# Kernel tuning notes

Measured on AMD Instinct MI355X. Metric: run time of the kernel, lower is better.

## Reference

```python
import jax, jax.numpy as jnp
import numpy as np

D_MODEL = 1024
NUM_HEADS = 16
HEAD_DIM = D_MODEL // NUM_HEADS


def setup_inputs() -> dict:
    key = jax.random.key(0)
    ks = jax.random.split(key, 11)
    B, S = 4, 2048
    scale = 1.0 / np.sqrt(D_MODEL)
    inp = {
        'q': jax.random.normal(ks[0], (B, S, D_MODEL), jnp.float32),
        'k': jax.random.normal(ks[1], (B, S, D_MODEL), jnp.float32),
        'v': jax.random.normal(ks[2], (B, S, D_MODEL), jnp.float32),
        'Wq': jax.random.normal(ks[3], (D_MODEL, D_MODEL), jnp.float32) * scale,
        'bq': jnp.zeros((D_MODEL,), jnp.float32),
        'Wk': jax.random.normal(ks[4], (D_MODEL, D_MODEL), jnp.float32) * scale,
        'bk': jnp.zeros((D_MODEL,), jnp.float32),
        'Wv': jax.random.normal(ks[5], (D_MODEL, D_MODEL), jnp.float32) * scale,
        'bv': jnp.zeros((D_MODEL,), jnp.float32),
        'Wo': jax.random.normal(ks[6], (D_MODEL, D_MODEL), jnp.float32) * scale,
        'bo': jnp.zeros((D_MODEL,), jnp.float32),
    }
    return inp


def _split_heads(x):
    B, S, _ = x.shape
    return x.reshape(B, S, NUM_HEADS, HEAD_DIM).transpose(0, 2, 1, 3)  # [B,H,S,Dh]


def reference(q, k, v, Wq, bq, Wk, bk, Wv, bv, Wo, bo):
    Q = _split_heads(q @ Wq.T + bq)
    K = _split_heads(k @ Wk.T + bk)
    V = _split_heads(v @ Wv.T + bv)
    scores = jnp.einsum('bhqd,bhkd->bhqk', Q, K) / jnp.sqrt(jnp.float32(HEAD_DIM))
    attn = jax.nn.softmax(scores, axis=-1)
    out = jnp.einsum('bhqk,bhkd->bhqd', attn, V)  # [B,H,S,Dh]
    B, _, S, _ = out.shape
    out = out.transpose(0, 2, 1, 3).reshape(B, S, D_MODEL)
    return out @ Wo.T + bo
```

## Files before the change

kernel.cpp:

```cpp
#include <hip/hip_runtime.h>
#include <hip/hip_bf16.h>

#define DMODEL 1024
#define NHEADS 16
#define HDIM 64

typedef __bf16 bf16_t;
typedef __bf16 bf16x8 __attribute__((ext_vector_type(8)));
typedef float  f32x4  __attribute__((ext_vector_type(4)));
typedef float  f32x16 __attribute__((ext_vector_type(16)));

__device__ __forceinline__ bf16_t f2bf(float f) {
    unsigned int u = __builtin_bit_cast(unsigned int, f);
    u += 0x7FFF + ((u >> 16) & 1);
    unsigned short h = (unsigned short)(u >> 16);
    return __builtin_bit_cast(bf16_t, h);
}

__device__ __forceinline__ unsigned cvt_pk_bf16(float lo, float hi) {
    unsigned r;
    asm("v_cvt_pk_bf16_f32 %0, %1, %2" : "=v"(r) : "v"(lo), "v"(hi));
    return r;
}

__device__ __forceinline__ void gld_lds16(const bf16_t* g, bf16_t* l) {
    __builtin_amdgcn_global_load_lds(
        (const __attribute__((address_space(1))) unsigned int*)g,
        (__attribute__((address_space(3))) unsigned int*)l, 16, 0, 0);
}

__global__ __launch_bounds__(256) void cast_all(const float* __restrict__ Wq,
                                                const float* __restrict__ Wk,
                                                const float* __restrict__ Wv,
                                                const float* __restrict__ Wo,
                                                const float* __restrict__ q,
                                                const float* __restrict__ k,
                                                const float* __restrict__ v,
                                                bf16_t* __restrict__ Wall,
                                                bf16_t* __restrict__ qb,
                                                bf16_t* __restrict__ kb,
                                                bf16_t* __restrict__ vb,
                                                int nw, int na) {
    const int y = blockIdx.y;
    const float* s;
    bf16_t* d;
    int n;
    if (y == 0)      { s = Wq; d = Wall;               n = nw; }
    else if (y == 1) { s = Wk; d = Wall + (size_t)nw;  n = nw; }
    else if (y == 2) { s = Wv; d = Wall + 2 * (size_t)nw; n = nw; }
    else if (y == 3) { s = Wo; d = Wall + 3 * (size_t)nw; n = nw; }
    else if (y == 4) { s = q;  d = qb; n = na; }
    else if (y == 5) { s = k;  d = kb; n = na; }
    else             { s = v;  d = vb; n = na; }
    int i = blockIdx.x * blockDim.x + threadIdx.x;
    int stride = gridDim.x * blockDim.x;
    for (int idx = i * 4; idx < n; idx += stride * 4) {
        float4 vv = *reinterpret_cast<const float4*>(s + idx);
        uint2 u;
        u.x = cvt_pk_bf16(vv.x, vv.y);
        u.y = cvt_pk_bf16(vv.z, vv.w);
        *reinterpret_cast<uint2*>(d + idx) = u;
    }
}

__global__ __launch_bounds__(256) void gemm_qkv(const bf16_t* __restrict__ qb,
                                                const bf16_t* __restrict__ kb,
                                                const bf16_t* __restrict__ vb,
                                                const bf16_t* __restrict__ Wall,
                                                const float* __restrict__ bq,
                                                const float* __restrict__ bk,
                                                const float* __restrict__ bv,
                                                bf16_t* __restrict__ Qp,
                                                bf16_t* __restrict__ Kf,
                                                bf16_t* __restrict__ Vf,
                                                int M, float qscale, int S) {
    __shared__ bf16_t smemU[16384];
    const int K = DMODEL, N = DMODEL;
    const int z = blockIdx.z;
    const bf16_t* Ab = (z == 0) ? qb : (z == 1) ? kb : vb;
    const bf16_t* W = Wall + (size_t)z * DMODEL * DMODEL;
    const float* bias = (z == 0) ? bq : (z == 1) ? bk : bv;

    const int m0 = blockIdx.x * 128;
    const int n0 = blockIdx.y * 128;
    const int tid = threadIdx.x;
    const int wave = tid >> 6, lane = tid & 63;
    const int wm = wave >> 1, wn = wave & 1;
    const int lr = lane & 15, lg = lane >> 4;
    const int srow = lane >> 2, scol = (lane & 3) * 8;

    const bool swp = (z == 1);
    const int xo = (swp ? wn : wm) * 64;
    const int yo = (swp ? wm : wn) * 64;

    f32x4 acc[4][4];
#pragma unroll
    for (int i = 0; i < 4; ++i)
#pragma unroll
        for (int j = 0; j < 4; ++j) acc[i][j] = (f32x4){0.f, 0.f, 0.f, 0.f};

#pragma unroll
    for (int i = 0; i < 2; ++i) {
        int c = wave * 2 + i;
        gld_lds16(Ab + (size_t)(m0 + c * 16 + srow) * K + scol, smemU + c * 512);
        gld_lds16(W + (size_t)(n0 + c * 16 + srow) * K + scol, smemU + 8192 + c * 512);
    }
    asm volatile("s_waitcnt vmcnt(0)" ::: "memory");
    __syncthreads();

    const int nk = K / 32;
    for (int t = 0; t < nk; ++t) {
        const int cur = t & 1, nxt = cur ^ 1;
        const int ktn = (t + 1) * 32;
        if (t + 1 < nk) {
#pragma unroll
            for (int i = 0; i < 2; ++i) {
                int c = wave * 2 + i;
                gld_lds16(Ab + (size_t)(m0 + c * 16 + srow) * K + ktn + scol,
                          smemU + nxt * 4096 + c * 512);
                gld_lds16(W + (size_t)(n0 + c * 16 + srow) * K + ktn + scol,
                          smemU + 8192 + nxt * 4096 + c * 512);
            }
        }
        const bf16_t* Xs = smemU + (swp ? 8192 : 0) + cur * 4096;
        const bf16_t* Ys = smemU + (swp ? 0 : 8192) + cur * 4096;
        bf16x8 X[4], Y[4];
#pragma unroll
        for (int i = 0; i < 4; ++i)
            X[i] = *reinterpret_cast<const bf16x8*>(&Xs[(xo + i * 16 + lr) * 32 + lg * 8]);
#pragma unroll
        for (int j = 0; j < 4; ++j)
            Y[j] = *reinterpret_cast<const bf16x8*>(&Ys[(yo + j * 16 + lr) * 32 + lg * 8]);
#pragma unroll
        for (int i = 0; i < 4; ++i)
#pragma unroll
            for (int j = 0; j < 4; ++j)
                acc[i][j] = __builtin_amdgcn_mfma_f32_16x16x32_bf16(X[i], Y[j], acc[i][j], 0, 0, 0);
        asm volatile("s_waitcnt vmcnt(0)" ::: "memory");
        __syncthreads();
    }

    if (z == 0) {
#pragma unroll
        for (int i = 0; i < 4; ++i) {
            int row = m0 + wm * 64 + i * 16 + lg * 4;
#pragma unroll
            for (int j = 0; j < 4; ++j) {
                int col = n0 + wn * 64 + j * 16 + lr;
                float bv_ = bias[col];
#pragma unroll
                for (int r = 0; r < 4; ++r)
                    Qp[(size_t)(row + r) * N + col] = f2bf((acc[i][j][r] + bv_) * qscale);
            }
        }
    } else {
        const int key0 = m0 + wm * 64;
        const int b_ = key0 / S;
        const int t_ = (key0 % S) >> 6;
        const int h  = (n0 + wn * 64) >> 6;
        bf16_t* bounce = smemU + wave * 4096;
        if (z == 1) {
#pragma unroll
            for (int i = 0; i < 4; ++i) {
                int d0 = i * 16 + lg * 4;
                float4 bv4 = *reinterpret_cast<const float4*>(bias + h * 64 + d0);
#pragma unroll
                for (int j = 0; j < 4; ++j) {
                    uint2 u;
                    u.x = cvt_pk_bf16(acc[i][j][0] + bv4.x, acc[i][j][1] + bv4.y);
                    u.y = cvt_pk_bf16(acc[i][j][2] + bv4.z, acc[i][j][3] + bv4.w);
                    int key5 = (j & 1) * 16 + lr;
                    int off = ((j >> 1) * 4 + i) * 512 + key5 * 8 + (lg >> 1) * 256 + (lg & 1) * 4;
                    *reinterpret_cast<uint2*>(bounce + off) = u;
                }
            }
        } else {
#pragma unroll
            for (int j = 0; j < 4; ++j) {
                int dl = (j & 1) * 16 + lr;
                int gd = j >> 1;
                float bv_ = bias[h * 64 + j * 16 + lr];
#pragma unroll
                for (int i = 0; i < 4; ++i) {
                    uint2 u;
                    u.x = cvt_pk_bf16(acc[i][j][0] + bv_, acc[i][j][1] + bv_);
                    u.y = cvt_pk_bf16(acc[i][j][2] + bv_, acc[i][j][3] + bv_);
                    int off = (gd * 4 + i) * 512 + dl * 8 + (lg >> 1) * 256 + (lg & 1) * 4;
                    *reinterpret_cast<uint2*>(bounce + off) = u;
                }
            }
        }
        bf16_t* gout = ((z == 1) ? Kf : Vf)
                     + (size_t)(b_ * NHEADS + h) * ((size_t)S * HDIM) + (size_t)(t_ * 8) * 512;
#pragma unroll
        for (int c = 0; c < 8; ++c) {
            bf16x8 vv = *reinterpret_cast<const bf16x8*>(bounce + c * 512 + lane * 8);
            *reinterpret_cast<bf16x8*>(gout + c * 512 + lane * 8) = vv;
        }
    }
}

__global__ __launch_bounds__(256) void gemm_out(const bf16_t* __restrict__ Ab,
                                                const bf16_t* __restrict__ W,
                                                const float* __restrict__ bias,
                                                float* __restrict__ Cout,
                                                int M, int N, int K) {
    __shared__ bf16_t Asmem[2][128 * 32];
    __shared__ bf16_t Bsmem[2][128 * 32];
    const int m0 = blockIdx.x * 128;
    const int n0 = blockIdx.y * 128;
    const int tid = threadIdx.x;
    const int wave = tid >> 6, lane = tid & 63;
    const int wm = wave >> 1, wn = wave & 1;
    const int lr = lane & 15, lg = lane >> 4;
    const int srow = lane >> 2, scol = (lane & 3) * 8;

    f32x4 acc[4][4];
#pragma unroll
    for (int mi = 0; mi < 4; ++mi)
#pragma unroll
        for (int ni = 0; ni < 4; ++ni) acc[mi][ni] = (f32x4){0.f, 0.f, 0.f, 0.f};

#pragma unroll
    for (int i = 0; i < 2; ++i) {
        int c = wave * 2 + i;
        gld_lds16(Ab + (size_t)(m0 + c * 16 + srow) * K + scol, &Asmem[0][c * 512]);
        gld_lds16(W + (size_t)(n0 + c * 16 + srow) * K + scol, &Bsmem[0][c * 512]);
    }
    asm volatile("s_waitcnt vmcnt(0)" ::: "memory");
    __syncthreads();

    const int nk = K / 32;
    for (int t = 0; t < nk; ++t) {
        const int cur = t & 1, nxt = cur ^ 1;
        const int ktn = (t + 1) * 32;
        if (t + 1 < nk) {
#pragma unroll
            for (int i = 0; i < 2; ++i) {
                int c = wave * 2 + i;
                gld_lds16(Ab + (size_t)(m0 + c * 16 + srow) * K + ktn + scol, &Asmem[nxt][c * 512]);
                gld_lds16(W + (size_t)(n0 + c * 16 + srow) * K + ktn + scol, &Bsmem[nxt][c * 512]);
            }
        }
        bf16x8 af[4], bfr[4];
#pragma unroll
        for (int mi = 0; mi < 4; ++mi)
            af[mi] = *reinterpret_cast<const bf16x8*>(&Asmem[cur][(wm * 64 + mi * 16 + lr) * 32 + lg * 8]);
#pragma unroll
        for (int ni = 0; ni < 4; ++ni)
            bfr[ni] = *reinterpret_cast<const bf16x8*>(&Bsmem[cur][(wn * 64 + ni * 16 + lr) * 32 + lg * 8]);
#pragma unroll
        for (int mi = 0; mi < 4; ++mi)
#pragma unroll
            for (int ni = 0; ni < 4; ++ni)
                acc[mi][ni] = __builtin_amdgcn_mfma_f32_16x16x32_bf16(af[mi], bfr[ni], acc[mi][ni], 0, 0, 0);
        asm volatile("s_waitcnt vmcnt(0)" ::: "memory");
        __syncthreads();
    }

#pragma unroll
    for (int mi = 0; mi < 4; ++mi) {
        int row = m0 + wm * 64 + mi * 16 + lg * 4;
#pragma unroll
        for (int ni = 0; ni < 4; ++ni) {
            int col = n0 + wn * 64 + ni * 16 + lr;
            float bv = bias[col];
#pragma unroll
            for (int r = 0; r < 4; ++r)
                Cout[(size_t)(row + r) * N + col] = acc[mi][ni][r] + bv;
        }
    }
}

__global__ __launch_bounds__(256, 2) void attn_kernel(const bf16_t* __restrict__ Qp,
                                                      const bf16_t* __restrict__ KfG,
                                                      const bf16_t* __restrict__ VfG,
                                                      bf16_t* __restrict__ AO, int S) {
    const int tid = threadIdx.x;
    const int wave = tid >> 6, lane = tid & 63;
    const int ql = lane & 31;
    const int hi = lane >> 5;
    const int bh = blockIdx.x;
    const int b = bh >> 4, h = bh & 15;
    const int qt = blockIdx.y;
    const size_t base = ((size_t)b * S) * DMODEL + (size_t)h * HDIM;
    const size_t fbase = (size_t)bh * ((size_t)S * HDIM);

    const int qrow = qt * 128 + wave * 32 + ql;
    bf16x8 qf[4];
#pragma unroll
    for (int kc = 0; kc < 4; ++kc)
        qf[kc] = *reinterpret_cast<const bf16x8*>(Qp + base + (size_t)qrow * DMODEL + kc * 16 + hi * 8);

    f32x16 o0{}, o1{};
    float l_r = 0.f;

    const bf16_t* Kf = KfG + fbase;
    const bf16_t* Vf = VfG + fbase;
    const int le = lane * 8;

    const int NT = S / 64;
    for (int t = 0; t < NT; ++t) {
        const bf16_t* kt = Kf + t * 4096;
        const bf16_t* vt = Vf + t * 4096;
        bf16x8 kf0[4], kf1[4], vf0[4], vf1[4];
#pragma unroll
        for (int c = 0; c < 4; ++c) {
            kf0[c] = *reinterpret_cast<const bf16x8*>(kt + c * 512 + le);
            kf1[c] = *reinterpret_cast<const bf16x8*>(kt + 2048 + c * 512 + le);
            vf0[c] = *reinterpret_cast<const bf16x8*>(vt + c * 512 + le);
            vf1[c] = *reinterpret_cast<const bf16x8*>(vt + 2048 + c * 512 + le);
        }

        f32x16 s0{}, s1{};
        __builtin_amdgcn_s_setprio(1);
#pragma unroll
        for (int kc = 0; kc < 4; ++kc)
            s0 = __builtin_amdgcn_mfma_f32_32x32x16_bf16(kf0[kc], qf[kc], s0, 0, 0, 0);
#pragma unroll
        for (int kc = 0; kc < 4; ++kc)
            s1 = __builtin_amdgcn_mfma_f32_32x32x16_bf16(kf1[kc], qf[kc], s1, 0, 0, 0);
        __builtin_amdgcn_s_setprio(0);

#pragma unroll
        for (int r = 0; r < 16; ++r) {
            s0[r] = __builtin_amdgcn_exp2f(s0[r]);
            s1[r] = __builtin_amdgcn_exp2f(s1[r]);
        }
        float a4[8];
#pragma unroll
        for (int j = 0; j < 8; ++j)
            a4[j] = (s0[2 * j] + s0[2 * j + 1]) + (s1[2 * j] + s1[2 * j + 1]);
        float a2[4];
#pragma unroll
        for (int j = 0; j < 4; ++j) a2[j] = a4[2 * j] + a4[2 * j + 1];
        l_r += (a2[0] + a2[1]) + (a2[2] + a2[3]);

        unsigned w[8][2];
#pragma unroll
        for (int j = 0; j < 4; ++j) {
            w[j][0] = cvt_pk_bf16(s0[4 * j], s0[4 * j + 1]);
            w[j][1] = cvt_pk_bf16(s0[4 * j + 2], s0[4 * j + 3]);
            w[4 + j][0] = cvt_pk_bf16(s1[4 * j], s1[4 * j + 1]);
            w[4 + j][1] = cvt_pk_bf16(s1[4 * j + 2], s1[4 * j + 3]);
        }

#pragma unroll
        for (int kq = 0; kq < 4; ++kq) {
            unsigned own0 = hi ? w[2 * kq + 1][0] : w[2 * kq][0];
            unsigned own1 = hi ? w[2 * kq + 1][1] : w[2 * kq][1];
            unsigned y0 = hi ? w[2 * kq][0] : w[2 * kq + 1][0];
            unsigned y1 = hi ? w[2 * kq][1] : w[2 * kq + 1][1];
            y0 = (unsigned)__shfl_xor((int)y0, 32, 64);
            y1 = (unsigned)__shfl_xor((int)y1, 32, 64);
            union { unsigned u[4]; bf16x8 v; } pb;
            pb.u[0] = hi ? y0 : own0;
            pb.u[1] = hi ? y1 : own1;
            pb.u[2] = hi ? own0 : y0;
            pb.u[3] = hi ? own1 : y1;
            __builtin_amdgcn_s_setprio(1);
            o0 = __builtin_amdgcn_mfma_f32_32x32x16_bf16(vf0[kq], pb.v, o0, 0, 0, 0);
            o1 = __builtin_amdgcn_mfma_f32_32x32x16_bf16(vf1[kq], pb.v, o1, 0, 0, 0);
            __builtin_amdgcn_s_setprio(0);
        }
    }

    float l_all = l_r + __shfl_xor(l_r, 32, 64);
    float inv = 1.f / l_all;
    bf16_t* Ao = AO + base + (size_t)qrow * DMODEL;
#pragma unroll
    for (int j = 0; j < 4; ++j) {
        uint2 u0, u1;
        u0.x = cvt_pk_bf16(o0[4 * j] * inv, o0[4 * j + 1] * inv);
        u0.y = cvt_pk_bf16(o0[4 * j + 2] * inv, o0[4 * j + 3] * inv);
        *reinterpret_cast<uint2*>(Ao + 8 * j + 4 * hi) = u0;
        u1.x = cvt_pk_bf16(o1[4 * j] * inv, o1[4 * j + 1] * inv);
        u1.y = cvt_pk_bf16(o1[4 * j + 2] * inv, o1[4 * j + 3] * inv);
        *reinterpret_cast<uint2*>(Ao + 32 + 8 * j + 4 * hi) = u1;
    }
}

extern "C" void kernel_launch(void* const* d_in, const int* in_sizes, int n_in,
                              void* d_out, int out_size, void* d_ws, size_t ws_size,
                              hipStream_t stream) {
    const float* q  = (const float*)d_in[0];
    const float* k  = (const float*)d_in[1];
    const float* v  = (const float*)d_in[2];
    const float* Wq = (const float*)d_in[3];
    const float* bq = (const float*)d_in[4];
    const float* Wk = (const float*)d_in[5];
    const float* bk = (const float*)d_in[6];
    const float* Wv = (const float*)d_in[7];
    const float* bv = (const float*)d_in[8];
    const float* Wo = (const float*)d_in[9];
    const float* bo = (const float*)d_in[10];

    const int M = in_sizes[0] / DMODEL;
    const int S = 2048;
    const int B = M / S;

    bf16_t* ws  = (bf16_t*)d_ws;
    const size_t WSZ = (size_t)DMODEL * DMODEL;
    const size_t MSZ = (size_t)M * DMODEL;
    bf16_t* Wqb = ws;
    bf16_t* Wob = Wqb + 3 * WSZ;
    bf16_t* Qp  = Wob + WSZ;
    bf16_t* Kf  = Qp + MSZ;
    bf16_t* Vf  = Kf + MSZ;
    bf16_t* shX = Vf + MSZ;
    bf16_t* qb  = (bf16_t*)d_out;
    bf16_t* kb  = qb + MSZ;
    bf16_t* vb  = shX;
    bf16_t* AO  = shX;

    cast_all<<<dim3(2048, 7), 256, 0, stream>>>(Wq, Wk, Wv, Wo, q, k, v,
                                                ws, qb, kb, vb,
                                                DMODEL * DMODEL, M * DMODEL);

    const float qscale = 0.125f * 1.44269504088896f;
    gemm_qkv<<<dim3(M / 128, DMODEL / 128, 3), 256, 0, stream>>>(
        qb, kb, vb, Wqb, bq, bk, bv, Qp, Kf, Vf, M, qscale, S);

    attn_kernel<<<dim3(B * NHEADS, S / 128), 256, 0, stream>>>(Qp, Kf, Vf, AO, S);

    gemm_out<<<dim3(M / 128, DMODEL / 128), 256, 0, stream>>>(
        AO, Wob, bo, (float*)d_out, M, DMODEL, DMODEL);
}
```

Measured before the change: 226.8 us.

## Process two query row tiles per wave to reuse K/V fragments

Each wave now handles 64 query rows (two 32-row groups) instead of 32, so every K and V fragment loaded from global memory feeds twice as many MFMAs. The grid's query-tile dimension is halved to match, and V loads move into the PV loop to limit register pressure. This cuts K/V load traffic per unit of compute, but doubles the accumulator registers, which may reduce occupancy under launch_bounds(256,2) or cause spills. It also leaves only 512 blocks.

```diff
diff --git a/kernel.cpp b/kernel.cpp
--- a/kernel.cpp
+++ b/kernel.cpp
@@ -286,14 +286,17 @@
     const size_t base = ((size_t)b * S) * DMODEL + (size_t)h * HDIM;
     const size_t fbase = (size_t)bh * ((size_t)S * HDIM);
 
-    const int qrow = qt * 128 + wave * 32 + ql;
-    bf16x8 qf[4];
-#pragma unroll
-    for (int kc = 0; kc < 4; ++kc)
-        qf[kc] = *reinterpret_cast<const bf16x8*>(Qp + base + (size_t)qrow * DMODEL + kc * 16 + hi * 8);
-
-    f32x16 o0{}, o1{};
-    float l_r = 0.f;
+    const int qrowA = qt * 256 + wave * 32 + ql;
+    const int qrowB = qrowA + 128;
+    bf16x8 qfA[4], qfB[4];
+#pragma unroll
+    for (int kc = 0; kc < 4; ++kc) {
+        qfA[kc] = *reinterpret_cast<const bf16x8*>(Qp + base + (size_t)qrowA * DMODEL + kc * 16 + hi * 8);
+        qfB[kc] = *reinterpret_cast<const bf16x8*>(Qp + base + (size_t)qrowB * DMODEL + kc * 16 + hi * 8);
+    }
+
+    f32x16 oA0{}, oA1{}, oB0{}, oB1{};
+    float lA = 0.f, lB = 0.f;
 
     const bf16_t* Kf = KfG + fbase;
     const bf16_t* Vf = VfG + fbase;
@@ -303,80 +306,124 @@
     for (int t = 0; t < NT; ++t) {
         const bf16_t* kt = Kf + t * 4096;
         const bf16_t* vt = Vf + t * 4096;
-        bf16x8 kf0[4], kf1[4], vf0[4], vf1[4];
+
+        bf16x8 kf0[4], kf1[4];
 #pragma unroll
         for (int c = 0; c < 4; ++c) {
             kf0[c] = *reinterpret_cast<const bf16x8*>(kt + c * 512 + le);
             kf1[c] = *reinterpret_cast<const bf16x8*>(kt + 2048 + c * 512 + le);
-            vf0[c] = *reinterpret_cast<const bf16x8*>(vt + c * 512 + le);
-            vf1[c] = *reinterpret_cast<const bf16x8*>(vt + 2048 + c * 512 + le);
-        }
-
-        f32x16 s0{}, s1{};
+        }
+        f32x16 sA0{}, sA1{}, sB0{}, sB1{};
         __builtin_amdgcn_s_setprio(1);
 #pragma unroll
-        for (int kc = 0; kc < 4; ++kc)
-            s0 = __builtin_amdgcn_mfma_f32_32x32x16_bf16(kf0[kc], qf[kc], s0, 0, 0, 0);
-#pragma unroll
-        for (int kc = 0; kc < 4; ++kc)
-            s1 = __builtin_amdgcn_mfma_f32_32x32x16_bf16(kf1[kc], qf[kc], s1, 0, 0, 0);
+        for (int kc = 0; kc < 4; ++kc) {
+            sA0 = __builtin_amdgcn_mfma_f32_32x32x16_bf16(kf0[kc], qfA[kc], sA0, 0, 0, 0);
+            sB0 = __builtin_amdgcn_mfma_f32_32x32x16_bf16(kf0[kc], qfB[kc], sB0, 0, 0, 0);
+            sA1 = __builtin_amdgcn_mfma_f32_32x32x16_bf16(kf1[kc], qfA[kc], sA1, 0, 0, 0);
+            sB1 = __builtin_amdgcn_mfma_f32_32x32x16_bf16(kf1[kc], qfB[kc], sB1, 0, 0, 0);
+        }
         __builtin_amdgcn_s_setprio(0);
 
 #pragma unroll
         for (int r = 0; r < 16; ++r) {
-            s0[r] = __builtin_amdgcn_exp2f(s0[r]);
-            s1[r] = __builtin_amdgcn_exp2f(s1[r]);
-        }
-        float a4[8];
-#pragma unroll
-        for (int j = 0; j < 8; ++j)
-            a4[j] = (s0[2 * j] + s0[2 * j + 1]) + (s1[2 * j] + s1[2 * j + 1]);
-        float a2[4];
-#pragma unroll
-        for (int j = 0; j < 4; ++j) a2[j] = a4[2 * j] + a4[2 * j + 1];
-        l_r += (a2[0] + a2[1]) + (a2[2] + a2[3]);
-
-        unsigned w[8][2];
+            sA0[r] = __builtin_amdgcn_exp2f(sA0[r]);
+            sA1[r] = __builtin_amdgcn_exp2f(sA1[r]);
+            sB0[r] = __builtin_amdgcn_exp2f(sB0[r]);
+            sB1[r] = __builtin_amdgcn_exp2f(sB1[r]);
+        }
+        {
+            float a4[8], b4[8];
+#pragma unroll
+            for (int j = 0; j < 8; ++j) {
+                a4[j] = (sA0[2 * j] + sA0[2 * j + 1]) + (sA1[2 * j] + sA1[2 * j + 1]);
+                b4[j] = (sB0[2 * j] + sB0[2 * j + 1]) + (sB1[2 * j] + sB1[2 * j + 1]);
+            }
+            float a2[4], b2[4];
+#pragma unroll
+            for (int j = 0; j < 4; ++j) {
+                a2[j] = a4[2 * j] + a4[2 * j + 1];
+                b2[j] = b4[2 * j] + b4[2 * j + 1];
+            }
+            lA += (a2[0] + a2[1]) + (a2[2] + a2[3]);
+            lB += (b2[0] + b2[1]) + (b2[2] + b2[3]);
+        }
+
+        unsigned wA[8][2], wB[8][2];
 #pragma unroll
         for (int j = 0; j < 4; ++j) {
-            w[j][0] = cvt_pk_bf16(s0[4 * j], s0[4 * j + 1]);
-            w[j][1] = cvt_pk_bf16(s0[4 * j + 2], s0[4 * j + 3]);
-            w[4 + j][0] = cvt_pk_bf16(s1[4 * j], s1[4 * j + 1]);
-            w[4 + j][1] = cvt_pk_bf16(s1[4 * j + 2], s1[4 * j + 3]);
+            wA[j][0] = cvt_pk_bf16(sA0[4 * j], sA0[4 * j + 1]);
+            wA[j][1] = cvt_pk_bf16(sA0[4 * j + 2], sA0[4 * j + 3]);
+            wA[4 + j][0] = cvt_pk_bf16(sA1[4 * j], sA1[4 * j + 1]);
+            wA[4 + j][1] = cvt_pk_bf16(sA1[4 * j + 2], sA1[4 * j + 3]);
+            wB[j][0] = cvt_pk_bf16(sB0[4 * j], sB0[4 * j + 1]);
+            wB[j][1] = cvt_pk_bf16(sB0[4 * j + 2], sB0[4 * j + 3]);
+            wB[4 + j][0] = cvt_pk_bf16(sB1[4 * j], sB1[4 * j + 1]);
+            wB[4 + j][1] = cvt_pk_bf16(sB1[4 * j + 2], sB1[4 * j + 3]);
         }
 
 #pragma unroll
         for (int kq = 0; kq < 4; ++kq) {
-            unsigned own0 = hi ? w[2 * kq + 1][0] : w[2 * kq][0];
-            unsigned own1 = hi ? w[2 * kq + 1][1] : w[2 * kq][1];
-            unsigned y0 = hi ? w[2 * kq][0] : w[2 * kq + 1][0];
-            unsigned y1 = hi ? w[2 * kq][1] : w[2 * kq + 1][1];
-            y0 = (unsigned)__shfl_xor((int)y0, 32, 64);
-            y1 = (unsigned)__shfl_xor((int)y1, 32, 64);
-            union { unsigned u[4]; bf16x8 v; } pb;
-            pb.u[0] = hi ? y0 : own0;
-            pb.u[1] = hi ? y1 : own1;
-            pb.u[2] = hi ? own0 : y0;
-            pb.u[3] = hi ? own1 : y1;
+            bf16x8 vf0 = *reinterpret_cast<const bf16x8*>(vt + kq * 512 + le);
+            bf16x8 vf1 = *reinterpret_cast<const bf16x8*>(vt + 2048 + kq * 512 + le);
+            unsigned oA0_ = hi ? wA[2 * kq + 1][0] : wA[2 * kq][0];
+            unsigned oA1_ = hi ? wA[2 * kq + 1][1] : wA[2 * kq][1];
+            unsigned yA0 = hi ? wA[2 * kq][0] : wA[2 * kq + 1][0];
+            unsigned yA1 = hi ? wA[2 * kq][1] : wA[2 * kq + 1][1];
+            yA0 = (unsigned)__shfl_xor((int)yA0, 32, 64);
+            yA1 = (unsigned)__shfl_xor((int)yA1, 32, 64);
+            unsigned oB0_ = hi ? wB[2 * kq + 1][0] : wB[2 * kq][0];
+            unsigned oB1_ = hi ? wB[2 * kq + 1][1] : wB[2 * kq][1];
+            unsigned yB0 = hi ? wB[2 * kq][0] : wB[2 * kq + 1][0];
+            unsigned yB1 = hi ? wB[2 * kq][1] : wB[2 * kq + 1][1];
+            yB0 = (unsigned)__shfl_xor((int)yB0, 32, 64);
+            yB1 = (unsigned)__shfl_xor((int)yB1, 32, 64);
+            union { unsigned u[4]; bf16x8 v; } pbA, pbB;
+            pbA.u[0] = hi ? yA0 : oA0_;
+            pbA.u[1] = hi ? yA1 : oA1_;
+            pbA.u[2] = hi ? oA0_ : yA0;
+            pbA.u[3] = hi ? oA1_ : yA1;
+            pbB.u[0] = hi ? yB0 : oB0_;
+            pbB.u[1] = hi ? yB1 : oB1_;
+            pbB.u[2] = hi ? oB0_ : yB0;
+            pbB.u[3] = hi ? oB1_ : yB1;
             __builtin_amdgcn_s_setprio(1);
-            o0 = __builtin_amdgcn_mfma_f32_32x32x16_bf16(vf0[kq], pb.v, o0, 0, 0, 0);
-            o1 = __builtin_amdgcn_mfma_f32_32x32x16_bf16(vf1[kq], pb.v, o1, 0, 0, 0);
+            oA0 = __builtin_amdgcn_mfma_f32_32x32x16_bf16(vf0, pbA.v, oA0, 0, 0, 0);
+            oB0 = __builtin_amdgcn_mfma_f32_32x32x16_bf16(vf0, pbB.v, oB0, 0, 0, 0);
+            oA1 = __builtin_amdgcn_mfma_f32_32x32x16_bf16(vf1, pbA.v, oA1, 0, 0, 0);
+            oB1 = __builtin_amdgcn_mfma_f32_32x32x16_bf16(vf1, pbB.v, oB1, 0, 0, 0);
             __builtin_amdgcn_s_setprio(0);
         }
     }
 
-    float l_all = l_r + __shfl_xor(l_r, 32, 64);
-    float inv = 1.f / l_all;
-    bf16_t* Ao = AO + base + (size_t)qrow * DMODEL;
-#pragma unroll
-    for (int j = 0; j < 4; ++j) {
-        uint2 u0, u1;
-        u0.x = cvt_pk_bf16(o0[4 * j] * inv, o0[4 * j + 1] * inv);
-        u0.y = cvt_pk_bf16(o0[4 * j + 2] * inv, o0[4 * j + 3] * inv);
-        *reinterpret_cast<uint2*>(Ao + 8 * j + 4 * hi) = u0;
-        u1.x = cvt_pk_bf16(o1[4 * j] * inv, o1[4 * j + 1] * inv);
-        u1.y = cvt_pk_bf16(o1[4 * j + 2] * inv, o1[4 * j + 3] * inv);
-        *reinterpret_cast<uint2*>(Ao + 32 + 8 * j + 4 * hi) = u1;
+    {
+        float l_all = lA + __shfl_xor(lA, 32, 64);
+        float inv = 1.f / l_all;
+        bf16_t* Ao = AO + base + (size_t)qrowA * DMODEL;
+#pragma unroll
+        for (int j = 0; j < 4; ++j) {
+            uint2 u0, u1;
+            u0.x = cvt_pk_bf16(oA0[4 * j] * inv, oA0[4 * j + 1] * inv);
+            u0.y = cvt_pk_bf16(oA0[4 * j + 2] * inv, oA0[4 * j + 3] * inv);
+            *reinterpret_cast<uint2*>(Ao + 8 * j + 4 * hi) = u0;
+            u1.x = cvt_pk_bf16(oA1[4 * j] * inv, oA1[4 * j + 1] * inv);
+            u1.y = cvt_pk_bf16(oA1[4 * j + 2] * inv, oA1[4 * j + 3] * inv);
+            *reinterpret_cast<uint2*>(Ao + 32 + 8 * j + 4 * hi) = u1;
+        }
+    }
+    {
+        float l_all = lB + __shfl_xor(lB, 32, 64);
+        float inv = 1.f / l_all;
+        bf16_t* Ao = AO + base + (size_t)qrowB * DMODEL;
+#pragma unroll
+        for (int j = 0; j < 4; ++j) {
+            uint2 u0, u1;
+            u0.x = cvt_pk_bf16(oB0[4 * j] * inv, oB0[4 * j + 1] * inv);
+            u0.y = cvt_pk_bf16(oB0[4 * j + 2] * inv, oB0[4 * j + 3] * inv);
+            *reinterpret_cast<uint2*>(Ao + 8 * j + 4 * hi) = u0;
+            u1.x = cvt_pk_bf16(oB1[4 * j] * inv, oB1[4 * j + 1] * inv);
+            u1.y = cvt_pk_bf16(oB1[4 * j + 2] * inv, oB1[4 * j + 3] * inv);
+            *reinterpret_cast<uint2*>(Ao + 32 + 8 * j + 4 * hi) = u1;
+        }
     }
 }
 
@@ -421,7 +468,7 @@
     gemm_qkv<<<dim3(M / 128, DMODEL / 128, 3), 256, 0, stream>>>(
         qb, kb, vb, Wqb, bq, bk, bv, Qp, Kf, Vf, M, qscale, S);
 
-    attn_kernel<<<dim3(B * NHEADS, S / 128), 256, 0, stream>>>(Qp, Kf, Vf, AO, S);
+    attn_kernel<<<dim3(B * NHEADS, S / 256), 256, 0, stream>>>(Qp, Kf, Vf, AO, S);
 
     gemm_out<<<dim3(M / 128, DMODEL / 128), 256, 0, stream>>>(
         AO, Wob, bo, (float*)d_out, M, DMODEL, DMODEL);
```

New measurement: 223.1 us. About the same (-1.6%).

## Software-pipeline attention loop: prefetch K and overlap QK of next tile with softmax-PV

Applied to the files above, without the earlier changes.

Restructures the flash-attention inner loop into a two-stage ping-pong pipeline. K tiles are prefetched two iterations ahead, and the QK^T MFMAs for tile t+1 are issued before the exp/PV work for tile t, so the matrix and vector units can overlap. V loads move inline next to the PV MFMAs. Out-of-range prefetches are clamped to the last tile, and the loop assumes an even tile count. The extra live score and K register sets raise VGPR pressure, which may lower occupancy.

```diff
diff --git a/kernel.cpp b/kernel.cpp
--- a/kernel.cpp
+++ b/kernel.cpp
@@ -298,39 +298,36 @@
     const bf16_t* Kf = KfG + fbase;
     const bf16_t* Vf = VfG + fbase;
     const int le = lane * 8;
-
     const int NT = S / 64;
-    for (int t = 0; t < NT; ++t) {
-        const bf16_t* kt = Kf + t * 4096;
-        const bf16_t* vt = Vf + t * 4096;
-        bf16x8 kf0[4], kf1[4], vf0[4], vf1[4];
+
+    auto loadK = [&](int t, bf16x8 (&k0)[4], bf16x8 (&k1)[4]) {
+        const bf16_t* kt = Kf + (size_t)min(t, NT - 1) * 4096;
 #pragma unroll
         for (int c = 0; c < 4; ++c) {
-            kf0[c] = *reinterpret_cast<const bf16x8*>(kt + c * 512 + le);
-            kf1[c] = *reinterpret_cast<const bf16x8*>(kt + 2048 + c * 512 + le);
-            vf0[c] = *reinterpret_cast<const bf16x8*>(vt + c * 512 + le);
-            vf1[c] = *reinterpret_cast<const bf16x8*>(vt + 2048 + c * 512 + le);
-        }
-
-        f32x16 s0{}, s1{};
+            k0[c] = *reinterpret_cast<const bf16x8*>(kt + c * 512 + le);
+            k1[c] = *reinterpret_cast<const bf16x8*>(kt + 2048 + c * 512 + le);
+        }
+    };
+    auto qk = [&](bf16x8 (&k0)[4], bf16x8 (&k1)[4], f32x16& s0v, f32x16& s1v) {
         __builtin_amdgcn_s_setprio(1);
 #pragma unroll
-        for (int kc = 0; kc < 4; ++kc)
-            s0 = __builtin_amdgcn_mfma_f32_32x32x16_bf16(kf0[kc], qf[kc], s0, 0, 0, 0);
-#pragma unroll
-        for (int kc = 0; kc < 4; ++kc)
-            s1 = __builtin_amdgcn_mfma_f32_32x32x16_bf16(kf1[kc], qf[kc], s1, 0, 0, 0);
+        for (int kc = 0; kc < 4; ++kc) {
+            s0v = __builtin_amdgcn_mfma_f32_32x32x16_bf16(k0[kc], qf[kc], s0v, 0, 0, 0);
+            s1v = __builtin_amdgcn_mfma_f32_32x32x16_bf16(k1[kc], qf[kc], s1v, 0, 0, 0);
+        }
         __builtin_amdgcn_s_setprio(0);
-
+    };
+    auto smpv = [&](f32x16& s0v, f32x16& s1v, int t) {
+        const bf16_t* vt = Vf + (size_t)t * 4096;
 #pragma unroll
         for (int r = 0; r < 16; ++r) {
-            s0[r] = __builtin_amdgcn_exp2f(s0[r]);
-            s1[r] = __builtin_amdgcn_exp2f(s1[r]);
+            s0v[r] = __builtin_amdgcn_exp2f(s0v[r]);
+            s1v[r] = __builtin_amdgcn_exp2f(s1v[r]);
         }
         float a4[8];
 #pragma unroll
         for (int j = 0; j < 8; ++j)
-            a4[j] = (s0[2 * j] + s0[2 * j + 1]) + (s1[2 * j] + s1[2 * j + 1]);
+            a4[j] = (s0v[2 * j] + s0v[2 * j + 1]) + (s1v[2 * j] + s1v[2 * j + 1]);
         float a2[4];
 #pragma unroll
         for (int j = 0; j < 4; ++j) a2[j] = a4[2 * j] + a4[2 * j + 1];
@@ -339,14 +336,15 @@
         unsigned w[8][2];
 #pragma unroll
         for (int j = 0; j < 4; ++j) {
-            w[j][0] = cvt_pk_bf16(s0[4 * j], s0[4 * j + 1]);
-            w[j][1] = cvt_pk_bf16(s0[4 * j + 2], s0[4 * j + 3]);
-            w[4 + j][0] = cvt_pk_bf16(s1[4 * j], s1[4 * j + 1]);
-            w[4 + j][1] = cvt_pk_bf16(s1[4 * j + 2], s1[4 * j + 3]);
-        }
-
+            w[j][0] = cvt_pk_bf16(s0v[4 * j], s0v[4 * j + 1]);
+            w[j][1] = cvt_pk_bf16(s0v[4 * j + 2], s0v[4 * j + 3]);
+            w[4 + j][0] = cvt_pk_bf16(s1v[4 * j], s1v[4 * j + 1]);
+            w[4 + j][1] = cvt_pk_bf16(s1v[4 * j + 2], s1v[4 * j + 3]);
+        }
 #pragma unroll
         for (int kq = 0; kq < 4; ++kq) {
+            bf16x8 vf0 = *reinterpret_cast<const bf16x8*>(vt + kq * 512 + le);
+            bf16x8 vf1 = *reinterpret_cast<const bf16x8*>(vt + 2048 + kq * 512 + le);
             unsigned own0 = hi ? w[2 * kq + 1][0] : w[2 * kq][0];
             unsigned own1 = hi ? w[2 * kq + 1][1] : w[2 * kq][1];
             unsigned y0 = hi ? w[2 * kq][0] : w[2 * kq + 1][0];
@@ -359,10 +357,30 @@
             pb.u[2] = hi ? own0 : y0;
             pb.u[3] = hi ? own1 : y1;
             __builtin_amdgcn_s_setprio(1);
-            o0 = __builtin_amdgcn_mfma_f32_32x32x16_bf16(vf0[kq], pb.v, o0, 0, 0, 0);
-            o1 = __builtin_amdgcn_mfma_f32_32x32x16_bf16(vf1[kq], pb.v, o1, 0, 0, 0);
+            o0 = __builtin_amdgcn_mfma_f32_32x32x16_bf16(vf0, pb.v, o0, 0, 0, 0);
+            o1 = __builtin_amdgcn_mfma_f32_32x32x16_bf16(vf1, pb.v, o1, 0, 0, 0);
             __builtin_amdgcn_s_setprio(0);
         }
+    };
+
+    bf16x8 kfE0[4], kfE1[4], kfO0[4], kfO1[4];
+    f32x16 sE0{}, sE1{}, sO0{}, sO1{};
+
+    loadK(0, kfE0, kfE1);
+    qk(kfE0, kfE1, sE0, sE1);
+    loadK(1, kfO0, kfO1);
+
+    for (int t = 0; t < NT; t += 2) {
+        loadK(t + 2, kfE0, kfE1);
+        sO0 = (f32x16){};
+        sO1 = (f32x16){};
+        qk(kfO0, kfO1, sO0, sO1);
+        smpv(sE0, sE1, t);
+        loadK(t + 3, kfO0, kfO1);
+        sE0 = (f32x16){};
+        sE1 = (f32x16){};
+        qk(kfE0, kfE1, sE0, sE1);
+        smpv(sO0, sO1, t + 1);
     }
 
     float l_all = l_r + __shfl_xor(l_r, 32, 64);
```

New measurement: 232.6 us. +2.6%, slower.
